# Performance work log

Measured on AMD Instinct MI355X. Metric: run time of the kernel, lower is better.

Reference implementation:

```python
import jax, jax.numpy as jnp
import numpy as np

N, D, K = 8192, 4096, 8
F_HID = D // 4  # 1024


def setup_inputs() -> dict:
    key = jax.random.key(0)
    ks = jax.random.split(key, 8)
    s1 = 1.0 / np.sqrt(2 * D)
    s2 = 1.0 / np.sqrt(F_HID)
    sr = 1.0 / np.sqrt(D)
    return {
        "h_anchor": jax.random.normal(ks[0], (N, D), jnp.float32),
        "h_mask": jax.random.normal(ks[1], (N, D), jnp.float32),
        "Wr": jax.random.normal(ks[2], (K, D), jnp.float32) * sr,
        "br": jnp.zeros((K,), jnp.float32),
        "W1": jax.random.normal(ks[3], (K, F_HID, 2 * D), jnp.float32) * s1,
        "b1": jnp.zeros((K, F_HID), jnp.float32),
        "W2": jax.random.normal(ks[4], (K, D, F_HID), jnp.float32) * s2,
        "b2": jnp.zeros((K, D), jnp.float32),
    }


def reference(h_anchor, h_mask, Wr, br, W1, b1, W2, b2):
    # routing weights: softmax(h_mask @ Wr^T + br) -> [N, K]
    weights = jax.nn.softmax(h_mask @ Wr.T + br, axis=-1)
    # conditioned input: [N, 2D]
    conditioned = jnp.concatenate([h_anchor, h_mask], axis=-1)
    # all-expert first GEMM: [K, N, F]
    h1 = jnp.einsum("nc,kfc->knf", conditioned, W1) + b1[:, None, :]
    h1 = jax.nn.gelu(h1, approximate=False)  # torch nn.GELU default = exact erf
    # second GEMM: [K, N, D]
    expert_out = jnp.einsum("knf,kdf->knd", h1, W2) + b2[:, None, :]
    # softmax-weighted combine over experts -> [N, D]
    return jnp.einsum("knd,nk->nd", expert_out, weights)
```

## Files before the change

kernel.cpp:

```cpp
#include <hip/hip_runtime.h>
#include <hip/hip_bf16.h>
#include <math.h>

typedef __bf16 bf16_t;
typedef __bf16 bf16x8 __attribute__((ext_vector_type(8)));
typedef float  f32x4  __attribute__((ext_vector_type(4)));

#define AS1 __attribute__((address_space(1)))
#define AS3 __attribute__((address_space(3)))

__device__ __forceinline__ void gload_lds16(const bf16_t* g, char* l) {
  __builtin_amdgcn_global_load_lds((const AS1 void*)g, (AS3 void*)l, 16, 0, 0);
}

static constexpr int N_ROWS = 8192;
static constexpr int DDIM   = 4096;
static constexpr int KEXP   = 8;
static constexpr int FHID   = 1024;
static constexpr int KD     = 8192;

__global__ __launch_bounds__(256)
void routing_kernel(const float* __restrict__ hm, const float* __restrict__ Wr,
                    const float* __restrict__ br, float* __restrict__ wgt) {
  const int n = blockIdx.x;
  const int t = threadIdx.x;
  const int wid = t >> 6;
  const float4* row = (const float4*)(hm + (size_t)n * DDIM);
  float4 x[4];
#pragma unroll
  for (int j = 0; j < 4; ++j) x[j] = row[t + j * 256];
  __shared__ float red[KEXP][4];
  float part[KEXP];
#pragma unroll
  for (int k = 0; k < KEXP; ++k) {
    const float4* wr = (const float4*)(Wr + (size_t)k * DDIM);
    float s = 0.f;
#pragma unroll
    for (int j = 0; j < 4; ++j) {
      float4 w4 = wr[t + j * 256];
      s += x[j].x * w4.x + x[j].y * w4.y + x[j].z * w4.z + x[j].w * w4.w;
    }
#pragma unroll
    for (int off = 32; off > 0; off >>= 1) s += __shfl_down(s, off);
    part[k] = s;
  }
  if ((t & 63) == 0) {
#pragma unroll
    for (int k = 0; k < KEXP; ++k) red[k][wid] = part[k];
  }
  __syncthreads();
  if (t == 0) {
    float lg[KEXP];
    float mx = -1e30f;
#pragma unroll
    for (int k = 0; k < KEXP; ++k) {
      lg[k] = red[k][0] + red[k][1] + red[k][2] + red[k][3] + br[k];
      mx = fmaxf(mx, lg[k]);
    }
    float sum = 0.f;
#pragma unroll
    for (int k = 0; k < KEXP; ++k) { lg[k] = expf(lg[k] - mx); sum += lg[k]; }
    float inv = 1.f / sum;
#pragma unroll
    for (int k = 0; k < KEXP; ++k) wgt[(size_t)n * KEXP + k] = lg[k] * inv;
  }
}

__device__ __forceinline__ bf16x8 cvt8(float4 f0, float4 f1) {
  bf16x8 o;
  o[0] = (bf16_t)f0.x; o[1] = (bf16_t)f0.y; o[2] = (bf16_t)f0.z; o[3] = (bf16_t)f0.w;
  o[4] = (bf16_t)f1.x; o[5] = (bf16_t)f1.y; o[6] = (bf16_t)f1.z; o[7] = (bf16_t)f1.w;
  return o;
}

__global__ __launch_bounds__(256)
void conv_cond_kernel(const float* __restrict__ ha, const float* __restrict__ hm,
                      bf16_t* __restrict__ A) {
  size_t c = (size_t)blockIdx.x * 256 + threadIdx.x;
  int n   = (int)(c >> 10);
  int pos = ((int)c & 1023) * 8;
  const float* src = (pos < DDIM) ? ha + (size_t)n * DDIM + pos
                                  : hm + (size_t)n * DDIM + (pos - DDIM);
  float4 f0 = ((const float4*)src)[0];
  float4 f1 = ((const float4*)src)[1];
  *(bf16x8*)(A + c * 8) = cvt8(f0, f1);
}

__global__ __launch_bounds__(256)
void conv_cast_kernel(const float* __restrict__ in, bf16_t* __restrict__ out) {
  size_t c = (size_t)blockIdx.x * 256 + threadIdx.x;
  float4 f0 = ((const float4*)(in + c * 8))[0];
  float4 f1 = ((const float4*)(in + c * 8))[1];
  *(bf16x8*)(out + c * 8) = cvt8(f0, f1);
}

__global__ __launch_bounds__(256)
void conv_w2_kernel(const float* __restrict__ W2, bf16_t* __restrict__ B2) {
  size_t c = (size_t)blockIdx.x * 256 + threadIdx.x;
  int f8 = (int)(c & 127);
  int d  = (int)((c >> 7) & 4095);
  int k  = (int)(c >> 19);
  const float* src = W2 + ((size_t)k * DDIM + d) * FHID + f8 * 8;
  float4 f0 = ((const float4*)src)[0];
  float4 f1 = ((const float4*)src)[1];
  *(bf16x8*)(B2 + (size_t)d * KD + k * FHID + f8 * 8) = cvt8(f0, f1);
}

template <int MODE, int NCOLS>
__global__ __launch_bounds__(512, 2)
void gemm256_kernel(const bf16_t* __restrict__ Amat, const bf16_t* __restrict__ Bmat,
                    void* __restrict__ Cout, const float* __restrict__ bias,
                    const float* __restrict__ wgt) {
  constexpr int BM = 256, BN = 256, BK = 32;
  constexpr int NT = KD / BK;
  constexpr int BUFB = 32768;
  __shared__ char lds_raw[4 * BUFB];

  const int tid  = threadIdx.x;
  const int wid  = tid >> 6;
  const int lane = tid & 63;
  const int wr   = wid >> 2;
  const int wc   = wid & 3;

  constexpr int NBN    = NCOLS / BN;
  constexpr int NWIN_N = NBN / 16;
  const int bid = blockIdx.x;
  const int w   = bid >> 8;
  const int sl  = bid & 255;
  const int xcd = sl & 7;
  const int cu  = sl >> 3;
  const int wm  = w / NWIN_N, wn = w % NWIN_N;
  const int bm  = wm * 16 + ((xcd >> 1) << 2) + (cu & 3);
  const int bn  = wn * 16 + ((xcd & 1) << 3) + (cu >> 2);
  const int arow0 = bm * BM;
  const int brow0 = bn * BN;

  const bf16_t* srcA[2];
  const bf16_t* srcB[2];
  int dstA[2], dstB[2];
#pragma unroll
  for (int i = 0; i < 2; ++i) {
    int p    = i * 8192 + tid * 16;
    int l    = p ^ (((p >> 7) & 3) << 4);
    int lrow = l >> 6;
    int lcol = (l & 63) >> 1;
    srcA[i] = Amat + (size_t)(arow0 + lrow) * KD + lcol;
    srcB[i] = Bmat + (size_t)(brow0 + lrow) * KD + lcol;
    dstA[i] = i * 8192 + (wid << 10);
    dstB[i] = 16384 + dstA[i];
  }

  const int j = lane >> 4;
  int aoffB[8], boffB[4];
#pragma unroll
  for (int mi = 0; mi < 8; ++mi) {
    int row = wr * 128 + mi * 16 + (lane & 15);
    aoffB[mi] = row * 64 + ((j ^ ((row >> 1) & 3)) << 4);
  }
#pragma unroll
  for (int ni = 0; ni < 4; ++ni) {
    int row = wc * 64 + ni * 16 + (lane & 15);
    boffB[ni] = 16384 + row * 64 + ((j ^ ((row >> 1) & 3)) << 4);
  }

  f32x4 acc[8][4];
  f32x4 zero = {0.f, 0.f, 0.f, 0.f};
#pragma unroll
  for (int mi = 0; mi < 8; ++mi)
#pragma unroll
    for (int ni = 0; ni < 4; ++ni) acc[mi][ni] = zero;

#pragma unroll
  for (int pt = 0; pt < 3; ++pt) {
    char* base = lds_raw + pt * BUFB;
#pragma unroll
    for (int i = 0; i < 2; ++i) gload_lds16(srcA[i] + (size_t)pt * BK, base + dstA[i]);
#pragma unroll
    for (int i = 0; i < 2; ++i) gload_lds16(srcB[i] + (size_t)pt * BK, base + dstB[i]);
  }

  for (int t = 0; t < NT; ++t) {
    const int bufo = (t & 3) * BUFB;
    const int ts   = (t + 3) & (NT - 1);
    char* sbase = lds_raw + ((t + 3) & 3) * BUFB;

    asm volatile("s_waitcnt vmcnt(8)" ::: "memory");
    __builtin_amdgcn_s_barrier();

#pragma unroll
    for (int i = 0; i < 2; ++i) gload_lds16(srcA[i] + (size_t)ts * BK, sbase + dstA[i]);
#pragma unroll
    for (int i = 0; i < 2; ++i) gload_lds16(srcB[i] + (size_t)ts * BK, sbase + dstB[i]);

    bf16x8 a0[4], bb[4], a1[4];
#pragma unroll
    for (int mi = 0; mi < 4; ++mi)
      a0[mi] = *(const bf16x8*)(lds_raw + bufo + aoffB[mi]);
#pragma unroll
    for (int ni = 0; ni < 4; ++ni)
      bb[ni] = *(const bf16x8*)(lds_raw + bufo + boffB[ni]);
    __builtin_amdgcn_sched_barrier(0);
#pragma unroll
    for (int mi = 0; mi < 4; ++mi)
      a1[mi] = *(const bf16x8*)(lds_raw + bufo + aoffB[mi + 4]);
    __builtin_amdgcn_sched_barrier(0);

    asm volatile("s_waitcnt lgkmcnt(4)" ::: "memory");
    __builtin_amdgcn_sched_barrier(0);
    __builtin_amdgcn_s_setprio(1);
#pragma unroll
    for (int mi = 0; mi < 4; ++mi)
#pragma unroll
      for (int ni = 0; ni < 4; ++ni)
        acc[mi][ni] = __builtin_amdgcn_mfma_f32_16x16x32_bf16(a0[mi], bb[ni], acc[mi][ni], 0, 0, 0);
    __builtin_amdgcn_s_setprio(0);
    __builtin_amdgcn_sched_barrier(0);

    asm volatile("s_waitcnt lgkmcnt(0)" ::: "memory");
    __builtin_amdgcn_sched_barrier(0);
    __builtin_amdgcn_s_setprio(1);
#pragma unroll
    for (int mi = 0; mi < 4; ++mi)
#pragma unroll
      for (int ni = 0; ni < 4; ++ni)
        acc[mi + 4][ni] = __builtin_amdgcn_mfma_f32_16x16x32_bf16(a1[mi], bb[ni], acc[mi + 4][ni], 0, 0, 0);
    __builtin_amdgcn_s_setprio(0);
    __builtin_amdgcn_sched_barrier(0);
  }

  const int grow0 = arow0 + wr * 128 + ((lane >> 4) << 2);
  const int gcol0 = brow0 + wc * 64 + (lane & 15);

  if constexpr (MODE == 1) {
    bf16_t* __restrict__ H = (bf16_t*)Cout;
    const int kexp = brow0 >> 10;
#pragma unroll
    for (int mi = 0; mi < 8; ++mi) {
      float wn4[4];
#pragma unroll
      for (int r = 0; r < 4; ++r)
        wn4[r] = wgt[(size_t)(grow0 + mi * 16 + r) * KEXP + kexp];
#pragma unroll
      for (int ni = 0; ni < 4; ++ni) {
        int col = gcol0 + ni * 16;
        float bv = bias[col];
#pragma unroll
        for (int r = 0; r < 4; ++r) {
          int n = grow0 + mi * 16 + r;
          float x = acc[mi][ni][r] + bv;
          float g = 0.5f * x * (1.f + erff(x * 0.70710678118654752f));
          H[(size_t)n * KD + col] = (bf16_t)(g * wn4[r]);
        }
      }
    }
  } else {
    float* __restrict__ O = (float*)Cout;
    float bcol[4][KEXP];
#pragma unroll
    for (int ni = 0; ni < 4; ++ni)
#pragma unroll
      for (int k = 0; k < KEXP; ++k)
        bcol[ni][k] = bias[(size_t)k * NCOLS + gcol0 + ni * 16];
#pragma unroll
    for (int mi = 0; mi < 8; ++mi)
#pragma unroll
      for (int r = 0; r < 4; ++r) {
        int n = grow0 + mi * 16 + r;
        const float4* wp = (const float4*)(wgt + (size_t)n * KEXP);
        float4 wa = wp[0], wb = wp[1];
        float w8[KEXP] = {wa.x, wa.y, wa.z, wa.w, wb.x, wb.y, wb.z, wb.w};
#pragma unroll
        for (int ni = 0; ni < 4; ++ni) {
          float bb2 = 0.f;
#pragma unroll
          for (int k = 0; k < KEXP; ++k) bb2 += w8[k] * bcol[ni][k];
          O[(size_t)n * NCOLS + gcol0 + ni * 16] = acc[mi][ni][r] + bb2;
        }
      }
  }
}

extern "C" void kernel_launch(void* const* d_in, const int* in_sizes, int n_in,
                              void* d_out, int out_size, void* d_ws, size_t ws_size,
                              hipStream_t stream) {
  const float* h_anchor = (const float*)d_in[0];
  const float* h_mask   = (const float*)d_in[1];
  const float* Wr       = (const float*)d_in[2];
  const float* br       = (const float*)d_in[3];
  const float* W1       = (const float*)d_in[4];
  const float* b1       = (const float*)d_in[5];
  const float* W2       = (const float*)d_in[6];
  const float* b2       = (const float*)d_in[7];
  float* out = (float*)d_out;

  char* ws = (char*)d_ws;
  bf16_t* Abf  = (bf16_t*)(ws);
  bf16_t* W1bf = (bf16_t*)(ws + ((size_t)128 << 20));
  bf16_t* W2bf = (bf16_t*)(ws + ((size_t)256 << 20));
  bf16_t* H1s  = (bf16_t*)(ws + ((size_t)320 << 20));
  float*  wgt  = (float*) (ws + ((size_t)448 << 20));

  routing_kernel<<<N_ROWS, 256, 0, stream>>>(h_mask, Wr, br, wgt);
  conv_cond_kernel<<<(N_ROWS * KD / 8) / 256, 256, 0, stream>>>(h_anchor, h_mask, Abf);
  conv_cast_kernel<<<(KEXP * FHID * 2 * DDIM / 8) / 256, 256, 0, stream>>>(W1, W1bf);
  conv_w2_kernel<<<(KEXP * DDIM * FHID / 8) / 256, 256, 0, stream>>>(W2, W2bf);

  gemm256_kernel<1, 8192><<<(N_ROWS / 256) * (KD / 256), 512, 0, stream>>>(
      Abf, W1bf, (void*)H1s, b1, wgt);
  gemm256_kernel<2, 4096><<<(N_ROWS / 256) * (DDIM / 256), 512, 0, stream>>>(
      H1s, W2bf, (void*)out, b2, wgt);
}
```

Before: 1.641 ms.

## Double-buffer LDS fragment registers to overlap LDS reads with MFMA

Unrolls the main GEMM loop by two and keeps two register sets of A/B fragments. The next tile's LDS reads are issued between the MFMA groups of the current tile, instead of all being read at the start of each iteration. The global-load wait loosens from vmcnt(8) to vmcnt(4) so the next buffer is ready before it is prefetched. The goal is to hide LDS latency behind matrix-core work, at the cost of extra VGPR pressure that could reduce occupancy or cause spills.

```diff
diff --git a/kernel.cpp b/kernel.cpp
--- a/kernel.cpp
+++ b/kernel.cpp
@@ -179,54 +179,72 @@
     for (int i = 0; i < 2; ++i) gload_lds16(srcB[i] + (size_t)pt * BK, base + dstB[i]);
   }
 
-  for (int t = 0; t < NT; ++t) {
-    const int bufo = (t & 3) * BUFB;
-    const int ts   = (t + 3) & (NT - 1);
-    char* sbase = lds_raw + ((t + 3) & 3) * BUFB;
-
-    asm volatile("s_waitcnt vmcnt(8)" ::: "memory");
-    __builtin_amdgcn_s_barrier();
-
-#pragma unroll
-    for (int i = 0; i < 2; ++i) gload_lds16(srcA[i] + (size_t)ts * BK, sbase + dstA[i]);
-#pragma unroll
-    for (int i = 0; i < 2; ++i) gload_lds16(srcB[i] + (size_t)ts * BK, sbase + dstB[i]);
-
-    bf16x8 a0[4], bb[4], a1[4];
-#pragma unroll
-    for (int mi = 0; mi < 4; ++mi)
-      a0[mi] = *(const bf16x8*)(lds_raw + bufo + aoffB[mi]);
-#pragma unroll
-    for (int ni = 0; ni < 4; ++ni)
-      bb[ni] = *(const bf16x8*)(lds_raw + bufo + boffB[ni]);
-    __builtin_amdgcn_sched_barrier(0);
-#pragma unroll
-    for (int mi = 0; mi < 4; ++mi)
-      a1[mi] = *(const bf16x8*)(lds_raw + bufo + aoffB[mi + 4]);
-    __builtin_amdgcn_sched_barrier(0);
-
-    asm volatile("s_waitcnt lgkmcnt(4)" ::: "memory");
-    __builtin_amdgcn_sched_barrier(0);
-    __builtin_amdgcn_s_setprio(1);
-#pragma unroll
-    for (int mi = 0; mi < 4; ++mi)
-#pragma unroll
-      for (int ni = 0; ni < 4; ++ni)
-        acc[mi][ni] = __builtin_amdgcn_mfma_f32_16x16x32_bf16(a0[mi], bb[ni], acc[mi][ni], 0, 0, 0);
-    __builtin_amdgcn_s_setprio(0);
-    __builtin_amdgcn_sched_barrier(0);
-
-    asm volatile("s_waitcnt lgkmcnt(0)" ::: "memory");
-    __builtin_amdgcn_sched_barrier(0);
-    __builtin_amdgcn_s_setprio(1);
-#pragma unroll
-    for (int mi = 0; mi < 4; ++mi)
-#pragma unroll
-      for (int ni = 0; ni < 4; ++ni)
-        acc[mi + 4][ni] = __builtin_amdgcn_mfma_f32_16x16x32_bf16(a1[mi], bb[ni], acc[mi + 4][ni], 0, 0, 0);
-    __builtin_amdgcn_s_setprio(0);
-    __builtin_amdgcn_sched_barrier(0);
-  }
+  bf16x8 a0X[4], bbX[4], a1X[4];
+  bf16x8 a0Y[4], bbY[4], a1Y[4];
+
+  asm volatile("s_waitcnt vmcnt(8)" ::: "memory");
+  __builtin_amdgcn_s_barrier();
+#pragma unroll
+  for (int mi = 0; mi < 4; ++mi) a0X[mi] = *(const bf16x8*)(lds_raw + aoffB[mi]);
+  __builtin_amdgcn_sched_barrier(0);
+#pragma unroll
+  for (int ni = 0; ni < 4; ++ni) bbX[ni] = *(const bf16x8*)(lds_raw + boffB[ni]);
+  __builtin_amdgcn_sched_barrier(0);
+#pragma unroll
+  for (int mi = 0; mi < 4; ++mi) a1X[mi] = *(const bf16x8*)(lds_raw + aoffB[mi + 4]);
+  __builtin_amdgcn_sched_barrier(0);
+
+#define GBODY(T, A0C, BBC, A1C, A0N, BBN, A1N)                                          \
+  {                                                                                     \
+    const int ts   = ((T) + 3) & (NT - 1);                                              \
+    char* sbase = lds_raw + (((T) + 3) & 3) * BUFB;                                     \
+    char* nbase = lds_raw + (((T) + 1) & 3) * BUFB;                                     \
+    asm volatile("s_waitcnt vmcnt(4)" ::: "memory");               \
+    __builtin_amdgcn_s_barrier();                                                       \
+    _Pragma("unroll")                                                                   \
+    for (int i = 0; i < 2; ++i) gload_lds16(srcA[i] + (size_t)ts * BK, sbase + dstA[i]);\
+    _Pragma("unroll")                                                                   \
+    for (int i = 0; i < 2; ++i) gload_lds16(srcB[i] + (size_t)ts * BK, sbase + dstB[i]);\
+    __builtin_amdgcn_sched_barrier(0);                                                  \
+    asm volatile("s_waitcnt lgkmcnt(4)" ::: "memory");               \
+    __builtin_amdgcn_sched_barrier(0);                                                  \
+    __builtin_amdgcn_s_setprio(1);                                                      \
+    _Pragma("unroll")                                                                   \
+    for (int mi = 0; mi < 4; ++mi)                                                      \
+      _Pragma("unroll")                                                                 \
+      for (int ni = 0; ni < 4; ++ni)                                                    \
+        acc[mi][ni] = __builtin_amdgcn_mfma_f32_16x16x32_bf16(A0C[mi], BBC[ni],         \
+                                                              acc[mi][ni], 0, 0, 0);    \
+    __builtin_amdgcn_s_setprio(0);                                                      \
+    __builtin_amdgcn_sched_barrier(0);                                                  \
+    _Pragma("unroll")                                                                   \
+    for (int mi = 0; mi < 4; ++mi) A0N[mi] = *(const bf16x8*)(nbase + aoffB[mi]);       \
+    __builtin_amdgcn_sched_barrier(0);                                                  \
+    asm volatile("s_waitcnt lgkmcnt(4)" ::: "memory");                   \
+    __builtin_amdgcn_sched_barrier(0);                                                  \
+    __builtin_amdgcn_s_setprio(1);                                                      \
+    _Pragma("unroll")                                                                   \
+    for (int mi = 0; mi < 4; ++mi)                                                      \
+      _Pragma("unroll")                                                                 \
+      for (int ni = 0; ni < 4; ++ni)                                                    \
+        acc[mi + 4][ni] = __builtin_amdgcn_mfma_f32_16x16x32_bf16(A1C[mi], BBC[ni],     \
+                                                                 acc[mi + 4][ni],       \
+                                                                 0, 0, 0);              \
+    __builtin_amdgcn_s_setprio(0);                                                      \
+    __builtin_amdgcn_sched_barrier(0);                                                  \
+    _Pragma("unroll")                                                                   \
+    for (int ni = 0; ni < 4; ++ni) BBN[ni] = *(const bf16x8*)(nbase + boffB[ni]);       \
+    __builtin_amdgcn_sched_barrier(0);                                                  \
+    _Pragma("unroll")                                                                   \
+    for (int mi = 0; mi < 4; ++mi) A1N[mi] = *(const bf16x8*)(nbase + aoffB[mi + 4]);   \
+    __builtin_amdgcn_sched_barrier(0);                                                  \
+  }
+
+  for (int t = 0; t < NT; t += 2) {
+    GBODY(t,     a0X, bbX, a1X, a0Y, bbY, a1Y);
+    GBODY(t + 1, a0Y, bbY, a1Y, a0X, bbX, a1X);
+  }
+#undef GBODY
 
   const int grow0 = arow0 + wr * 128 + ((lane >> 4) << 2);
   const int gcol0 = brow0 + wc * 64 + (lane & 15);
```

After: 1.598 ms. -2.6%, faster.

## Restructure GEMM mainloop to BK=64 double buffer with phased 8-step schedule

Applied to the files above, without the earlier changes.

Replaces the 4-deep BK=32 LDS ring in the 256x256 GEMM with a 2-buffer BK=64 layout. Each k-tile is split into four phases that interleave half-tile global-to-LDS staging with LDS reads and MFMA bursts. Barriers are placed around each phase. The LDS swizzle changes to fit 128-byte rows, and a new XOR scheme selects the k sub-slice. The aim is fewer barrier and waitcnt round trips per FLOP and finer-grained overlap of loads with compute. In exchange, each phase adds two block barriers and the prefetch depth is shallower.

```diff
diff --git a/kernel.cpp b/kernel.cpp
--- a/kernel.cpp
+++ b/kernel.cpp
@@ -111,10 +111,9 @@
 void gemm256_kernel(const bf16_t* __restrict__ Amat, const bf16_t* __restrict__ Bmat,
                     void* __restrict__ Cout, const float* __restrict__ bias,
                     const float* __restrict__ wgt) {
-  constexpr int BM = 256, BN = 256, BK = 32;
-  constexpr int NT = KD / BK;
-  constexpr int BUFB = 32768;
-  __shared__ char lds_raw[4 * BUFB];
+  constexpr int BM = 256, BN = 256, BK = 64;
+  constexpr int NKT = KD / BK;
+  __shared__ char lds_raw[2 * 65536];
 
   const int tid  = threadIdx.x;
   const int wid  = tid >> 6;
@@ -135,32 +134,30 @@
   const int arow0 = bm * BM;
   const int brow0 = bn * BN;
 
-  const bf16_t* srcA[2];
-  const bf16_t* srcB[2];
-  int dstA[2], dstB[2];
-#pragma unroll
-  for (int i = 0; i < 2; ++i) {
-    int p    = i * 8192 + tid * 16;
-    int l    = p ^ (((p >> 7) & 3) << 4);
-    int lrow = l >> 6;
-    int lcol = (l & 63) >> 1;
-    srcA[i] = Amat + (size_t)(arow0 + lrow) * KD + lcol;
-    srcB[i] = Bmat + (size_t)(brow0 + lrow) * KD + lcol;
-    dstA[i] = i * 8192 + (wid << 10);
-    dstB[i] = 16384 + dstA[i];
-  }
+  const bf16_t* sA[2][2];
+  const bf16_t* sB[2][2];
+#pragma unroll
+  for (int h = 0; h < 2; ++h)
+#pragma unroll
+    for (int i = 0; i < 2; ++i) {
+      int p   = tid * 16 + i * 8192;
+      int l   = p ^ (((p >> 7) & 3) << 4) ^ (((p >> 9) & 1) << 6);
+      int row = l >> 7, c = l & 127;
+      sA[h][i] = Amat + (size_t)(arow0 + h * 128 + row) * KD + (c >> 1);
+      sB[h][i] = Bmat + (size_t)(brow0 + h * 128 + row) * KD + (c >> 1);
+    }
 
   const int j = lane >> 4;
-  int aoffB[8], boffB[4];
+  int aoff0[8], boff0[4];
 #pragma unroll
   for (int mi = 0; mi < 8; ++mi) {
     int row = wr * 128 + mi * 16 + (lane & 15);
-    aoffB[mi] = row * 64 + ((j ^ ((row >> 1) & 3)) << 4);
+    aoff0[mi] = row * 128 + ((j ^ (row & 3)) << 4) + (((row >> 2) & 1) << 6);
   }
 #pragma unroll
   for (int ni = 0; ni < 4; ++ni) {
     int row = wc * 64 + ni * 16 + (lane & 15);
-    boffB[ni] = 16384 + row * 64 + ((j ^ ((row >> 1) & 3)) << 4);
+    boff0[ni] = 32768 + row * 128 + ((j ^ (row & 3)) << 4) + (((row >> 2) & 1) << 6);
   }
 
   f32x4 acc[8][4];
@@ -170,63 +167,70 @@
 #pragma unroll
     for (int ni = 0; ni < 4; ++ni) acc[mi][ni] = zero;
 
-#pragma unroll
-  for (int pt = 0; pt < 3; ++pt) {
-    char* base = lds_raw + pt * BUFB;
-#pragma unroll
-    for (int i = 0; i < 2; ++i) gload_lds16(srcA[i] + (size_t)pt * BK, base + dstA[i]);
-#pragma unroll
-    for (int i = 0; i < 2; ++i) gload_lds16(srcB[i] + (size_t)pt * BK, base + dstB[i]);
-  }
-
-  for (int t = 0; t < NT; ++t) {
-    const int bufo = (t & 3) * BUFB;
-    const int ts   = (t + 3) & (NT - 1);
-    char* sbase = lds_raw + ((t + 3) & 3) * BUFB;
-
-    asm volatile("s_waitcnt vmcnt(8)" ::: "memory");
-    __builtin_amdgcn_s_barrier();
-
-#pragma unroll
-    for (int i = 0; i < 2; ++i) gload_lds16(srcA[i] + (size_t)ts * BK, sbase + dstA[i]);
-#pragma unroll
-    for (int i = 0; i < 2; ++i) gload_lds16(srcB[i] + (size_t)ts * BK, sbase + dstB[i]);
-
-    bf16x8 a0[4], bb[4], a1[4];
-#pragma unroll
-    for (int mi = 0; mi < 4; ++mi)
-      a0[mi] = *(const bf16x8*)(lds_raw + bufo + aoffB[mi]);
-#pragma unroll
-    for (int ni = 0; ni < 4; ++ni)
-      bb[ni] = *(const bf16x8*)(lds_raw + bufo + boffB[ni]);
-    __builtin_amdgcn_sched_barrier(0);
-#pragma unroll
-    for (int mi = 0; mi < 4; ++mi)
-      a1[mi] = *(const bf16x8*)(lds_raw + bufo + aoffB[mi + 4]);
-    __builtin_amdgcn_sched_barrier(0);
-
-    asm volatile("s_waitcnt lgkmcnt(4)" ::: "memory");
-    __builtin_amdgcn_sched_barrier(0);
-    __builtin_amdgcn_s_setprio(1);
-#pragma unroll
-    for (int mi = 0; mi < 4; ++mi)
-#pragma unroll
-      for (int ni = 0; ni < 4; ++ni)
-        acc[mi][ni] = __builtin_amdgcn_mfma_f32_16x16x32_bf16(a0[mi], bb[ni], acc[mi][ni], 0, 0, 0);
-    __builtin_amdgcn_s_setprio(0);
-    __builtin_amdgcn_sched_barrier(0);
-
-    asm volatile("s_waitcnt lgkmcnt(0)" ::: "memory");
-    __builtin_amdgcn_sched_barrier(0);
-    __builtin_amdgcn_s_setprio(1);
-#pragma unroll
-    for (int mi = 0; mi < 4; ++mi)
-#pragma unroll
-      for (int ni = 0; ni < 4; ++ni)
-        acc[mi + 4][ni] = __builtin_amdgcn_mfma_f32_16x16x32_bf16(a1[mi], bb[ni], acc[mi + 4][ni], 0, 0, 0);
-    __builtin_amdgcn_s_setprio(0);
-    __builtin_amdgcn_sched_barrier(0);
-  }
+#define STAGEA(H, TAU)                                                          \
+  { const size_t ko = (size_t)((TAU) & (NKT - 1)) * BK;                         \
+    char* db = lds_raw + (((TAU) & 1) * 65536) + (H) * 16384 + (wid << 10);     \
+    gload_lds16(sA[H][0] + ko, db);                                             \
+    gload_lds16(sA[H][1] + ko, db + 8192); }
+#define STAGEB(H, TAU)                                                          \
+  { const size_t ko = (size_t)((TAU) & (NKT - 1)) * BK;                         \
+    char* db = lds_raw + (((TAU) & 1) * 65536) + 32768 + (H) * 16384 + (wid << 10); \
+    gload_lds16(sB[H][0] + ko, db);                                             \
+    gload_lds16(sB[H][1] + ko, db + 8192); }
+
+  STAGEB(0, 0) STAGEA(0, 0) STAGEA(1, 0) STAGEB(1, 0) STAGEB(0, 1)
+  asm volatile("s_waitcnt vmcnt(2)" ::: "memory");
+  __builtin_amdgcn_s_barrier();
+
+  bf16x8 bb[4];
+
+#define PHASE(BUFO, HH, SS, STG, GATE)                                          \
+  {                                                                             \
+    bf16x8 aq[4];                                                               \
+    _Pragma("unroll")                                                           \
+    for (int mi = 0; mi < 4; ++mi)                                              \
+      aq[mi] = *(const bf16x8*)(lds_raw + (BUFO) +                              \
+                                (aoff0[(HH) * 4 + mi] ^ ((SS) * 64)));          \
+    if ((HH) == 0) {                                                            \
+      _Pragma("unroll")                                                         \
+      for (int ni = 0; ni < 4; ++ni)                                            \
+        bb[ni] = *(const bf16x8*)(lds_raw + (BUFO) +                            \
+                                  (boff0[ni] ^ ((SS) * 64)));                   \
+    }                                                                           \
+    STG;                                                                        \
+    __builtin_amdgcn_sched_barrier(0);                                          \
+    __builtin_amdgcn_s_barrier();                                               \
+    asm volatile("s_waitcnt lgkmcnt(0)" ::: "memory");                          \
+    __builtin_amdgcn_sched_barrier(0);                                          \
+    __builtin_amdgcn_s_setprio(1);                                              \
+    _Pragma("unroll")                                                           \
+    for (int mi = 0; mi < 4; ++mi)                                              \
+      _Pragma("unroll")                                                         \
+      for (int ni = 0; ni < 4; ++ni)                                            \
+        acc[(HH) * 4 + mi][ni] = __builtin_amdgcn_mfma_f32_16x16x32_bf16(       \
+            aq[mi], bb[ni], acc[(HH) * 4 + mi][ni], 0, 0, 0);                   \
+    __builtin_amdgcn_s_setprio(0);                                              \
+    __builtin_amdgcn_sched_barrier(0);                                          \
+    if (GATE) {                                                                 \
+      asm volatile("s_waitcnt vmcnt(2)" ::: "memory");                          \
+      __builtin_amdgcn_sched_barrier(0);                                        \
+    }                                                                           \
+    __builtin_amdgcn_s_barrier();                                               \
+  }
+
+  for (int t = 0; t < NKT; t += 2) {
+    PHASE(0,     0, 0, STAGEA(0, t + 1), 0)
+    PHASE(0,     1, 0, STAGEA(1, t + 1), 0)
+    PHASE(0,     0, 1, STAGEB(1, t + 1), 0)
+    PHASE(0,     1, 1, STAGEB(0, t + 2), 1)
+    PHASE(65536, 0, 0, STAGEA(0, t + 2), 0)
+    PHASE(65536, 1, 0, STAGEA(1, t + 2), 0)
+    PHASE(65536, 0, 1, STAGEB(1, t + 2), 0)
+    PHASE(65536, 1, 1, STAGEB(0, t + 3), 1)
+  }
+#undef PHASE
+#undef STAGEA
+#undef STAGEB
 
   const int grow0 = arow0 + wr * 128 + ((lane >> 4) << 2);
   const int gcol0 = brow0 + wc * 64 + (lane & 15);
```

Measured after the change: 1.534 ms. -6.5%, faster.
